# Optimization experiments

Hardware: AMD Instinct MI355X
Metric: run time of the kernel (lower is better)

The kernel has to match this reference:

```python
import jax, jax.numpy as jnp
import numpy as np

CHUNK = 64


def _rmsnorm(x, g, eps=1e-6):
    return x * jax.lax.rsqrt(jnp.mean(x * x, axis=-1, keepdims=True) + eps) * g


def setup_inputs() -> dict:
    key = jax.random.key(0)
    ks = jax.random.split(key, 8)
    B, L, D, N = 4, 4096, 512, 64
    s = 0.02
    return {
        'x': jax.random.normal(ks[0], (B, L, D), jnp.float32),
        'A_log': -jnp.ones((D,), jnp.float32) * jnp.log(2.0),
        'dt_bias': jnp.log(jnp.expm1(jax.random.uniform(ks[1], (D,), jnp.float32, 0.001, 0.1))),
        'D_skip': jnp.ones((D,), jnp.float32),
        'W_xproj': jax.random.normal(ks[2], (D, 2 * D), jnp.float32) * s,
        'b_xproj': jnp.zeros((2 * D,), jnp.float32),
        'W_B': jax.random.normal(ks[3], (D, N), jnp.float32) * s,
        'W_C': jax.random.normal(ks[4], (D, N), jnp.float32) * s,
        'W_dt': jax.random.normal(ks[5], (D, D), jnp.float32) * s,
        'g_Bnorm': jnp.ones((N,), jnp.float32),
        'g_Cnorm': jnp.ones((N,), jnp.float32),
        'g_outnorm': jnp.ones((D,), jnp.float32),
        'W_out': jax.random.normal(ks[6], (D, D), jnp.float32) * s,
        'b_out': jnp.zeros((D,), jnp.float32),
    }


def reference(x, A_log, dt_bias, D_skip, W_xproj, b_xproj, W_B, W_C, W_dt,
              g_Bnorm, g_Cnorm, g_outnorm, W_out, b_out):
    b, l, d = x.shape
    n = W_B.shape[1]
    p = CHUNK
    c = l // p  # L chosen divisible by chunk size (original pads otherwise)

    A = -jnp.exp(jnp.clip(A_log, -20.0, 2.0))  # (d,)
    xp = x @ W_xproj + b_xproj                  # (b,l,2d)
    x_bar, z = jnp.split(xp, 2, axis=-1)
    Bm = _rmsnorm(x_bar @ W_B, g_Bnorm)         # (b,l,n)
    Cm = _rmsnorm(x_bar @ W_C, g_Cnorm)         # (b,l,n)
    dt = jnp.clip(jax.nn.softplus(x_bar @ W_dt + dt_bias), 1e-4, 5.0)
    A_bar = jnp.exp(jnp.clip(dt * A, -20.0, 0.0))  # (b,l,d)

    to_chunks = lambda t: t.reshape(b, c, p, t.shape[-1]).transpose(1, 0, 2, 3)
    xc, Bc, Cc, Ac = map(to_chunks, (x_bar, Bm, Cm, A_bar))  # (c,b,p,*)
    mask = jnp.tril(jnp.ones((p, p), x.dtype))

    def process_chunk(prev_state, inputs):
        x_c, B_c, C_c, A_c = inputs
        log_a = jnp.log(jnp.clip(A_c, 1e-8, 1.0))
        la_cs = jnp.cumsum(log_a, axis=1)  # (b,p,d)
        # intra-chunk decay matrix M: (b,p,p,d)
        M = jnp.exp(la_cs[:, :, None, :] - la_cs[:, None, :, :]) * mask[None, :, :, None]
        BX = jnp.einsum('bpn,bpd->bpnd', B_c, x_c)
        state = jnp.einsum('bijd,bjnd->bind', M, BX)
        y_intra = jnp.einsum('bpn,bpnd->bpd', C_c, state)
        decay = jnp.exp(la_cs)
        y_inter = jnp.einsum('bpn,bpnd->bpd', C_c,
                             prev_state[:, None, :, :] * decay[:, :, None, :])
        y_c = y_intra + y_inter
        a_total = jnp.exp(la_cs[:, -1, :])             # (b,d)
        a_to_end = jnp.exp(la_cs[:, -1:, :] - la_cs)   # (b,p,d)
        chunk_state = jnp.einsum('bpn,bpd->bnd', B_c, x_c * a_to_end)
        new_state = prev_state * a_total[:, None, :] + chunk_state
        new_state = jnp.where(jnp.isfinite(new_state), new_state, 0.0)
        y_c = jnp.where(jnp.isfinite(y_c), y_c, 0.0)
        return new_state, y_c

    init = jnp.zeros((b, n, d), x.dtype)
    _, yc = jax.lax.scan(jax.checkpoint(process_chunk), init, (xc, Bc, Cc, Ac))
    y = yc.transpose(1, 0, 2, 3).reshape(b, l, d)
    y = jnp.where(jnp.isfinite(y), y, 0.0)
    y = y + D_skip * x_bar
    y = _rmsnorm(y, g_outnorm) * jax.nn.silu(z)
    return y @ W_out + b_out
```

## Files before the change

kernel.cpp:

```cpp
#include <hip/hip_runtime.h>
#include <hip/hip_bf16.h>
#include <math.h>

typedef __hip_bfloat16 bf16;
typedef __attribute__((ext_vector_type(8))) short short8;
typedef __attribute__((ext_vector_type(4))) float floatx4;

#define B_ 4
#define L_ 4096
#define D_ 512
#define M_ (B_*L_)

__device__ __forceinline__ float b2f(bf16 v){ return __bfloat162float(v); }
__device__ __forceinline__ bf16  f2b(float v){ return __float2bfloat16(v); }
__device__ __forceinline__ short f2bs(float v){ bf16 h = __float2bfloat16(v); short s; __builtin_memcpy(&s,&h,2); return s; }

#define GLD16(gp, lp) __builtin_amdgcn_global_load_lds( \
    (const __attribute__((address_space(1))) void*)(gp), \
    (__attribute__((address_space(3))) void*)(lp), 16, 0, 0)

__global__ __launch_bounds__(1024) void k_transpose(const float* __restrict__ src,
                                                    bf16* __restrict__ dst, int K, int N){
    __shared__ float tile[32][33];
    int n0 = blockIdx.x*32, k0 = blockIdx.y*32;
    int tx = threadIdx.x, ty = threadIdx.y;
    tile[ty][tx] = src[(size_t)(k0+ty)*N + n0+tx];
    __syncthreads();
    ((short*)dst)[(size_t)(n0+ty)*K + k0+tx] = f2bs(tile[tx][ty]);
}

__global__ __launch_bounds__(256) void k_cvt(const float* __restrict__ src,
                                             bf16* __restrict__ dst){
    size_t i = ((size_t)blockIdx.x*256 + threadIdx.x)*4;
    float4 v = *(const float4*)(src + i);
    short4 s; s.x=f2bs(v.x); s.y=f2bs(v.y); s.z=f2bs(v.z); s.w=f2bs(v.w);
    *(short4*)((short*)dst + i) = s;
}

template<int EPI>
__global__ __launch_bounds__(256) void k_gemm(const bf16* __restrict__ Ap,
        const bf16* __restrict__ Wt, const float* __restrict__ bias,
        const float* __restrict__ aux,
        float* __restrict__ o1, bf16* __restrict__ o2, bf16* __restrict__ o3){
    __shared__ short As[128*32];
    __shared__ short Bs[128*32];
    const int K = 512;
    int m0 = blockIdx.x*128, n0 = blockIdx.y*128;
    int tid=threadIdx.x, w=tid>>6, lane=tid&63;
    int wr=w>>1, wc=w&1, quad=lane>>4, r16=lane&15;
    floatx4 acc[4][4];
    #pragma unroll
    for (int i=0;i<4;i++)
        #pragma unroll
        for (int j=0;j<4;j++)
            #pragma unroll
            for (int e=0;e<4;e++) acc[i][j][e]=0.f;

    int c0 = tid, c1 = tid + 256;
    const short* Ab = (const short*)Ap + (size_t)m0*K;
    const short* Wb = (const short*)Wt + (size_t)n0*K;
    int r0 = c0>>2, g0 = (c0&3)*8;
    int r1 = c1>>2, g1 = (c1&3)*8;

    for (int k0=0;k0<K;k0+=32){
        GLD16(Ab + (size_t)r0*K + k0 + g0, &As[c0*8]);
        GLD16(Ab + (size_t)r1*K + k0 + g1, &As[c1*8]);
        GLD16(Wb + (size_t)r0*K + k0 + g0, &Bs[c0*8]);
        GLD16(Wb + (size_t)r1*K + k0 + g1, &Bs[c1*8]);
        __syncthreads();
        short8 af[4], bv[4];
        #pragma unroll
        for (int i=0;i<4;i++) af[i] = *(short8*)&As[(wr*64+i*16+r16)*32 + quad*8];
        #pragma unroll
        for (int j=0;j<4;j++) bv[j] = *(short8*)&Bs[(wc*64+j*16+r16)*32 + quad*8];
        #pragma unroll
        for (int i=0;i<4;i++)
            #pragma unroll
            for (int j=0;j<4;j++)
                acc[i][j] = __builtin_amdgcn_mfma_f32_16x16x32_bf16(af[i], bv[j], acc[i][j], 0,0,0);
        __syncthreads();
    }
    #pragma unroll
    for (int i=0;i<4;i++)
    #pragma unroll
    for (int j=0;j<4;j++)
    #pragma unroll
    for (int reg=0;reg<4;reg++){
        int gr = m0 + wr*64 + i*16 + quad*4 + reg;
        int gc = n0 + wc*64 + j*16 + r16;
        float v = acc[i][j][reg] + bias[gc];
        if (EPI==0){
            if (gc < 512){
                o1[(size_t)gr*512 + gc] = v;
                o2[(size_t)gr*512 + gc] = f2b(v);
            } else {
                o3[(size_t)gr*512 + (gc-512)] = f2b(v / (1.f + __expf(-v)));
            }
        } else if (EPI==1){
            float sp = (v > 15.f) ? v : log1pf(__expf(v));
            float dt = fminf(fmaxf(sp, 1e-4f), 5.f);
            float Ad = -__expf(fminf(fmaxf(aux[gc], -20.f), 2.f));
            o1[(size_t)gr*512 + gc] = fminf(fmaxf(dt*Ad, -18.420680743952367f), 0.f);
        } else {
            o1[(size_t)gr*512 + gc] = v;
        }
    }
}

__device__ __forceinline__ void gemm_tile_64x64(const bf16* __restrict__ Aptr,
                                                const bf16* __restrict__ Wt,
                                                int K, int m0, int n0,
                                                short (*As)[32], short (*Ns)[32],
                                                floatx4 acc[2][2]){
    int tid  = threadIdx.x;
    int w    = tid >> 6, lane = tid & 63;
    int wr   = w >> 1,  wc   = w & 1;
    int quad = lane >> 4, r16 = lane & 15;
    #pragma unroll
    for (int i=0;i<2;i++)
        #pragma unroll
        for (int j=0;j<2;j++)
            #pragma unroll
            for (int e=0;e<4;e++) acc[i][j][e] = 0.f;
    int lrow = tid >> 2, lkg = (tid & 3) * 8;
    for (int k0 = 0; k0 < K; k0 += 32){
        *(short8*)&As[lrow][lkg] = *(const short8*)((const short*)Aptr + (size_t)(m0+lrow)*K + k0 + lkg);
        *(short8*)&Ns[lrow][lkg] = *(const short8*)((const short*)Wt   + (size_t)(n0+lrow)*K + k0 + lkg);
        __syncthreads();
        short8 af[2], bfr[2];
        #pragma unroll
        for (int t=0;t<2;t++) af[t]  = *(short8*)&As[wr*32 + t*16 + r16][quad*8];
        #pragma unroll
        for (int t=0;t<2;t++) bfr[t] = *(short8*)&Ns[wc*32 + t*16 + r16][quad*8];
        #pragma unroll
        for (int i=0;i<2;i++)
            #pragma unroll
            for (int j=0;j<2;j++)
                acc[i][j] = __builtin_amdgcn_mfma_f32_16x16x32_bf16(af[i], bfr[j], acc[i][j], 0,0,0);
        __syncthreads();
    }
}

__global__ __launch_bounds__(256) void k_bcproj(const bf16* __restrict__ xbarh,
        const bf16* __restrict__ WtB, const bf16* __restrict__ WtC,
        const float* __restrict__ gB, const float* __restrict__ gC,
        float* __restrict__ Bm, float* __restrict__ Cm){
    __shared__ short As[64][32], Ns[64][32];
    __shared__ float Ls[64][64];
    __shared__ float rfac[64];
    const bf16* Wt = blockIdx.y ? WtC : WtB;
    const float* g = blockIdx.y ? gC  : gB;
    float* outp    = blockIdx.y ? Cm  : Bm;
    floatx4 acc[2][2];
    int m0 = blockIdx.x*64;
    gemm_tile_64x64(xbarh, Wt, 512, m0, 0, As, Ns, acc);
    int tid=threadIdx.x, w=tid>>6, lane=tid&63, wr=w>>1, wc=w&1, quad=lane>>4, r16=lane&15;
    #pragma unroll
    for (int i=0;i<2;i++)
    #pragma unroll
    for (int j=0;j<2;j++)
    #pragma unroll
    for (int reg=0;reg<4;reg++)
        Ls[wr*32+i*16+quad*4+reg][wc*32+j*16+r16] = acc[i][j][reg];
    __syncthreads();
    if (tid < 64){
        float ss = 0.f;
        #pragma unroll
        for (int cc=0;cc<64;cc++){ float t = Ls[tid][cc]; ss += t*t; }
        rfac[tid] = rsqrtf(ss*(1.f/64.f) + 1e-6f);
    }
    __syncthreads();
    #pragma unroll
    for (int it=0; it<16; it++){
        int idx = it*256 + tid;
        int r = idx >> 6, cc = idx & 63;
        outp[(size_t)(m0+r)*64 + cc] = Ls[r][cc] * rfac[r] * g[cc];
    }
}

__global__ __launch_bounds__(256) void k_pass1(const float* __restrict__ la,
        const float* __restrict__ xbar, const float* __restrict__ Bm,
        float* __restrict__ local, float* __restrict__ atot){
    __shared__ float Bs[64*64];
    int c=blockIdx.x, b=blockIdx.y, d=blockIdx.z*256+threadIdx.x;
    size_t rowbase=(size_t)b*L_+(size_t)c*64;
    size_t cb=(size_t)c*4+b;
    {
        const float4* src=(const float4*)(Bm + rowbase*64);
        float4* dst=(float4*)Bs;
        #pragma unroll
        for (int k=0;k<4;k++) dst[k*256+threadIdx.x]=src[k*256+threadIdx.x];
    }
    __syncthreads();
    float4 st[16];
    #pragma unroll
    for (int k=0;k<16;k++) st[k]=make_float4(0.f,0.f,0.f,0.f);
    float cs=0.f;
    size_t off0=rowbase*512+d;
    float la_n=la[off0], x_n=xbar[off0];
    #pragma unroll 2
    for (int i=0;i<64;i++){
        float lai=la_n, xi=x_n;
        if (i<63){ la_n=la[off0+(i+1)*512]; x_n=xbar[off0+(i+1)*512]; }
        float ai=__expf(lai);
        cs += lai;
        const float* Br=Bs+i*64;
        #pragma unroll
        for (int k=0;k<16;k++){
            float4 bv=*(const float4*)(Br+k*4);
            float4 s=st[k];
            s.x=fmaf(ai,s.x,bv.x*xi); s.y=fmaf(ai,s.y,bv.y*xi);
            s.z=fmaf(ai,s.z,bv.z*xi); s.w=fmaf(ai,s.w,bv.w*xi);
            st[k]=s;
        }
    }
    #pragma unroll
    for (int k=0;k<16;k++){
        size_t ob=(cb*64 + k*4)*512 + d;
        local[ob]      = st[k].x;
        local[ob+512]  = st[k].y;
        local[ob+1024] = st[k].z;
        local[ob+1536] = st[k].w;
    }
    atot[cb*512+d]=__expf(cs);
}

__global__ __launch_bounds__(256) void k_scan(float* __restrict__ local,
        const float* __restrict__ atot){
    int idx = blockIdx.x*256 + threadIdx.x;
    int d = idx & 511, n = (idx >> 9) & 63, b = idx >> 15;
    float s = 0.f;
    for (int c=0;c<64;c++){
        size_t cb = (size_t)c*4 + b;
        size_t off = (cb*64 + n)*512 + d;
        float v = local[off];
        local[off] = s;
        s = s * atot[cb*512 + d] + v;
        if (!isfinite(s)) s = 0.f;
    }
}

__global__ __launch_bounds__(256) void k_pass2(const float* __restrict__ la,
        const float* __restrict__ xbar, const float* __restrict__ Bm,
        const float* __restrict__ Cm, const float* __restrict__ Sprev,
        float* __restrict__ ybuf){
    __shared__ float Bs[64*64];
    __shared__ float Cs[64*64];
    int c=blockIdx.x, b=blockIdx.y, d=blockIdx.z*256+threadIdx.x;
    size_t rowbase=(size_t)b*L_+(size_t)c*64;
    size_t cb=(size_t)c*4+b;
    {
        const float4* sb=(const float4*)(Bm + rowbase*64);
        const float4* sc=(const float4*)(Cm + rowbase*64);
        float4* db=(float4*)Bs; float4* dc=(float4*)Cs;
        #pragma unroll
        for (int k=0;k<4;k++){
            db[k*256+threadIdx.x]=sb[k*256+threadIdx.x];
            dc[k*256+threadIdx.x]=sc[k*256+threadIdx.x];
        }
    }
    float4 st[16];
    #pragma unroll
    for (int k=0;k<16;k++){
        size_t ib=(cb*64 + k*4)*512 + d;
        st[k].x=Sprev[ib]; st[k].y=Sprev[ib+512];
        st[k].z=Sprev[ib+1024]; st[k].w=Sprev[ib+1536];
    }
    __syncthreads();
    size_t off0=rowbase*512+d;
    float la_n=la[off0], x_n=xbar[off0];
    #pragma unroll 2
    for (int i=0;i<64;i++){
        float lai=la_n, xi=x_n;
        if (i<63){ la_n=la[off0+(i+1)*512]; x_n=xbar[off0+(i+1)*512]; }
        float ai=__expf(lai);
        const float* Br=Bs+i*64;
        const float* Cr=Cs+i*64;
        float4 yv=make_float4(0.f,0.f,0.f,0.f);
        #pragma unroll
        for (int k=0;k<16;k++){
            float4 bv=*(const float4*)(Br+k*4);
            float4 cv=*(const float4*)(Cr+k*4);
            float4 s=st[k];
            s.x=fmaf(ai,s.x,bv.x*xi); s.y=fmaf(ai,s.y,bv.y*xi);
            s.z=fmaf(ai,s.z,bv.z*xi); s.w=fmaf(ai,s.w,bv.w*xi);
            st[k]=s;
            yv.x=fmaf(cv.x,s.x,yv.x); yv.y=fmaf(cv.y,s.y,yv.y);
            yv.z=fmaf(cv.z,s.z,yv.z); yv.w=fmaf(cv.w,s.w,yv.w);
        }
        float yo=(yv.x+yv.y)+(yv.z+yv.w);
        if (!isfinite(yo)) yo=0.f;
        ybuf[off0+i*512]=yo;
    }
}

__global__ __launch_bounds__(256) void k_outnorm(const float* __restrict__ y,
        const float* __restrict__ xbar, const float* __restrict__ Dskip,
        const float* __restrict__ g, const bf16* __restrict__ siluz,
        bf16* __restrict__ u){
    int wave = threadIdx.x >> 6, lane = threadIdx.x & 63;
    size_t row = (size_t)blockIdx.x*4 + wave;
    float v[8]; float ss = 0.f;
    #pragma unroll
    for (int j=0;j<8;j++){
        int d = j*64 + lane;
        float t = y[row*512 + d] + Dskip[d] * xbar[row*512 + d];
        v[j] = t; ss += t*t;
    }
    #pragma unroll
    for (int m=1;m<64;m<<=1) ss += __shfl_xor(ss, m, 64);
    float r = rsqrtf(ss*(1.f/512.f) + 1e-6f);
    #pragma unroll
    for (int j=0;j<8;j++){
        int d = j*64 + lane;
        u[row*512 + d] = f2b(v[j] * r * g[d] * b2f(siluz[row*512 + d]));
    }
}

extern "C" void kernel_launch(void* const* d_in, const int* in_sizes, int n_in,
                              void* d_out, int out_size, void* d_ws, size_t ws_size,
                              hipStream_t stream){
    const float* x       = (const float*)d_in[0];
    const float* A_log   = (const float*)d_in[1];
    const float* dt_bias = (const float*)d_in[2];
    const float* D_skip  = (const float*)d_in[3];
    const float* W_xproj = (const float*)d_in[4];
    const float* b_xproj = (const float*)d_in[5];
    const float* W_B     = (const float*)d_in[6];
    const float* W_C     = (const float*)d_in[7];
    const float* W_dt    = (const float*)d_in[8];
    const float* g_B     = (const float*)d_in[9];
    const float* g_C     = (const float*)d_in[10];
    const float* g_out   = (const float*)d_in[11];
    const float* W_out   = (const float*)d_in[12];
    const float* b_out   = (const float*)d_in[13];
    float* out = (float*)d_out;

    char* wp = (char*)d_ws;
    auto alloc = [&](size_t bytes)->char*{ char* p = wp; wp += (bytes + 255) & ~(size_t)255; return p; };
    float* xbar  = (float*)alloc((size_t)M_*512*4);
    bf16*  xh    = (bf16*) alloc((size_t)M_*512*2);
    bf16*  xbarh = (bf16*) alloc((size_t)M_*512*2);
    bf16*  siluz = (bf16*) alloc((size_t)M_*512*2);
    float* la    = (float*)alloc((size_t)M_*512*4);
    float* Bm    = (float*)alloc((size_t)M_*64*4);
    float* Cm    = (float*)alloc((size_t)M_*64*4);
    float* local = (float*)alloc((size_t)256*64*512*4);
    float* atot  = (float*)alloc((size_t)256*512*4);
    float* ybuf  = (float*)alloc((size_t)M_*512*4);
    bf16*  u     = (bf16*) alloc((size_t)M_*512*2);
    bf16*  WtX   = (bf16*) alloc((size_t)1024*512*2);
    bf16*  WtD   = (bf16*) alloc((size_t)512*512*2);
    bf16*  WtO   = (bf16*) alloc((size_t)512*512*2);
    bf16*  WtB   = (bf16*) alloc((size_t)64*512*2);
    bf16*  WtC   = (bf16*) alloc((size_t)64*512*2);

    dim3 tb(32,32);
    k_transpose<<<dim3(32,16), tb, 0, stream>>>(W_xproj, WtX, 512, 1024);
    k_transpose<<<dim3(16,16), tb, 0, stream>>>(W_dt,   WtD, 512, 512);
    k_transpose<<<dim3(16,16), tb, 0, stream>>>(W_out,  WtO, 512, 512);
    k_transpose<<<dim3(2,16),  tb, 0, stream>>>(W_B,    WtB, 512, 64);
    k_transpose<<<dim3(2,16),  tb, 0, stream>>>(W_C,    WtC, 512, 64);
    k_cvt      <<<M_*512/1024, 256, 0, stream>>>(x, xh);

    k_gemm<0> <<<dim3(128, 8), 256, 0, stream>>>(xh,    WtX, b_xproj, nullptr, xbar, xbarh, siluz);
    k_bcproj  <<<dim3(256, 2), 256, 0, stream>>>(xbarh, WtB, WtC, g_B, g_C, Bm, Cm);
    k_gemm<1> <<<dim3(128, 4), 256, 0, stream>>>(xbarh, WtD, dt_bias, A_log, la, nullptr, nullptr);
    k_pass1   <<<dim3(64,4,2), 256, 0, stream>>>(la, xbar, Bm, local, atot);
    k_scan    <<<512,          256, 0, stream>>>(local, atot);
    k_pass2   <<<dim3(64,4,2), 256, 0, stream>>>(la, xbar, Bm, Cm, local, ybuf);
    k_outnorm <<<M_/4,         256, 0, stream>>>(ybuf, xbar, D_skip, g_out, siluz, u);
    k_gemm<2> <<<dim3(128, 4), 256, 0, stream>>>(u,     WtO, b_out, nullptr, out, nullptr, nullptr);
}
```

Measured before the change: 372.4 us.

## Fuse B/C projections into main GEMM epilogue and pack two channels per scan thread

Replaces the separate 64x64-tile B/C projection kernel with one 128-wide GEMM launch over a concatenated B|C weight matrix. That launch applies both RMS norms in its epilogue using cross-lane shuffles. The chunk-scan pass1/pass2 kernels now give each thread two adjacent channels using float2 vectors, which halves the grid and doubles the state held in registers. This cuts launches and duplicate shared-memory loads of B/C, and may enable packed FP32 math. The cost is higher register pressure (128 state floats per thread) and half as many blocks in the scan kernels, which lowers occupancy.

```diff
diff --git a/kernel.cpp b/kernel.cpp
--- a/kernel.cpp
+++ b/kernel.cpp
@@ -5,6 +5,7 @@
 typedef __hip_bfloat16 bf16;
 typedef __attribute__((ext_vector_type(8))) short short8;
 typedef __attribute__((ext_vector_type(4))) float floatx4;
+typedef __attribute__((ext_vector_type(2))) float floatx2;
 
 #define B_ 4
 #define L_ 4096
@@ -14,6 +15,7 @@
 __device__ __forceinline__ float b2f(bf16 v){ return __bfloat162float(v); }
 __device__ __forceinline__ bf16  f2b(float v){ return __float2bfloat16(v); }
 __device__ __forceinline__ short f2bs(float v){ bf16 h = __float2bfloat16(v); short s; __builtin_memcpy(&s,&h,2); return s; }
+__device__ __forceinline__ floatx2 fx2(float v){ floatx2 r; r.x=v; r.y=v; return r; }
 
 #define GLD16(gp, lp) __builtin_amdgcn_global_load_lds( \
     (const __attribute__((address_space(1))) void*)(gp), \
@@ -41,7 +43,8 @@
 __global__ __launch_bounds__(256) void k_gemm(const bf16* __restrict__ Ap,
         const bf16* __restrict__ Wt, const float* __restrict__ bias,
         const float* __restrict__ aux,
-        float* __restrict__ o1, bf16* __restrict__ o2, bf16* __restrict__ o3){
+        float* __restrict__ o1, bf16* __restrict__ o2, bf16* __restrict__ o3,
+        float* __restrict__ o4){
     __shared__ short As[128*32];
     __shared__ short Bs[128*32];
     const int K = 512;
@@ -79,6 +82,29 @@
             for (int j=0;j<4;j++)
                 acc[i][j] = __builtin_amdgcn_mfma_f32_16x16x32_bf16(af[i], bv[j], acc[i][j], 0,0,0);
         __syncthreads();
+    }
+    if (EPI==3){
+        #pragma unroll
+        for (int i=0;i<4;i++)
+        #pragma unroll
+        for (int reg=0;reg<4;reg++){
+            float ss=0.f;
+            #pragma unroll
+            for (int j=0;j<4;j++){ float t=acc[i][j][reg]; ss+=t*t; }
+            #pragma unroll
+            for (int m=1;m<16;m<<=1) ss += __shfl_xor(ss, m, 64);
+            float rq = rsqrtf(ss*(1.f/64.f)+1e-6f);
+            int gr = m0 + wr*64 + i*16 + quad*4 + reg;
+            #pragma unroll
+            for (int j=0;j<4;j++){
+                int gc = wc*64 + j*16 + r16;
+                float gval = (gc<64) ? bias[gc] : aux[gc-64];
+                float v = acc[i][j][reg]*rq*gval;
+                if (gc<64) o1[(size_t)gr*64 + gc] = v;
+                else       o4[(size_t)gr*64 + (gc-64)] = v;
+            }
+        }
+        return;
     }
     #pragma unroll
     for (int i=0;i<4;i++)
@@ -107,82 +133,12 @@
     }
 }
 
-__device__ __forceinline__ void gemm_tile_64x64(const bf16* __restrict__ Aptr,
-                                                const bf16* __restrict__ Wt,
-                                                int K, int m0, int n0,
-                                                short (*As)[32], short (*Ns)[32],
-                                                floatx4 acc[2][2]){
-    int tid  = threadIdx.x;
-    int w    = tid >> 6, lane = tid & 63;
-    int wr   = w >> 1,  wc   = w & 1;
-    int quad = lane >> 4, r16 = lane & 15;
-    #pragma unroll
-    for (int i=0;i<2;i++)
-        #pragma unroll
-        for (int j=0;j<2;j++)
-            #pragma unroll
-            for (int e=0;e<4;e++) acc[i][j][e] = 0.f;
-    int lrow = tid >> 2, lkg = (tid & 3) * 8;
-    for (int k0 = 0; k0 < K; k0 += 32){
-        *(short8*)&As[lrow][lkg] = *(const short8*)((const short*)Aptr + (size_t)(m0+lrow)*K + k0 + lkg);
-        *(short8*)&Ns[lrow][lkg] = *(const short8*)((const short*)Wt   + (size_t)(n0+lrow)*K + k0 + lkg);
-        __syncthreads();
-        short8 af[2], bfr[2];
-        #pragma unroll
-        for (int t=0;t<2;t++) af[t]  = *(short8*)&As[wr*32 + t*16 + r16][quad*8];
-        #pragma unroll
-        for (int t=0;t<2;t++) bfr[t] = *(short8*)&Ns[wc*32 + t*16 + r16][quad*8];
-        #pragma unroll
-        for (int i=0;i<2;i++)
-            #pragma unroll
-            for (int j=0;j<2;j++)
-                acc[i][j] = __builtin_amdgcn_mfma_f32_16x16x32_bf16(af[i], bfr[j], acc[i][j], 0,0,0);
-        __syncthreads();
-    }
-}
-
-__global__ __launch_bounds__(256) void k_bcproj(const bf16* __restrict__ xbarh,
-        const bf16* __restrict__ WtB, const bf16* __restrict__ WtC,
-        const float* __restrict__ gB, const float* __restrict__ gC,
-        float* __restrict__ Bm, float* __restrict__ Cm){
-    __shared__ short As[64][32], Ns[64][32];
-    __shared__ float Ls[64][64];
-    __shared__ float rfac[64];
-    const bf16* Wt = blockIdx.y ? WtC : WtB;
-    const float* g = blockIdx.y ? gC  : gB;
-    float* outp    = blockIdx.y ? Cm  : Bm;
-    floatx4 acc[2][2];
-    int m0 = blockIdx.x*64;
-    gemm_tile_64x64(xbarh, Wt, 512, m0, 0, As, Ns, acc);
-    int tid=threadIdx.x, w=tid>>6, lane=tid&63, wr=w>>1, wc=w&1, quad=lane>>4, r16=lane&15;
-    #pragma unroll
-    for (int i=0;i<2;i++)
-    #pragma unroll
-    for (int j=0;j<2;j++)
-    #pragma unroll
-    for (int reg=0;reg<4;reg++)
-        Ls[wr*32+i*16+quad*4+reg][wc*32+j*16+r16] = acc[i][j][reg];
-    __syncthreads();
-    if (tid < 64){
-        float ss = 0.f;
-        #pragma unroll
-        for (int cc=0;cc<64;cc++){ float t = Ls[tid][cc]; ss += t*t; }
-        rfac[tid] = rsqrtf(ss*(1.f/64.f) + 1e-6f);
-    }
-    __syncthreads();
-    #pragma unroll
-    for (int it=0; it<16; it++){
-        int idx = it*256 + tid;
-        int r = idx >> 6, cc = idx & 63;
-        outp[(size_t)(m0+r)*64 + cc] = Ls[r][cc] * rfac[r] * g[cc];
-    }
-}
-
 __global__ __launch_bounds__(256) void k_pass1(const float* __restrict__ la,
         const float* __restrict__ xbar, const float* __restrict__ Bm,
         float* __restrict__ local, float* __restrict__ atot){
     __shared__ float Bs[64*64];
-    int c=blockIdx.x, b=blockIdx.y, d=blockIdx.z*256+threadIdx.x;
+    int c=blockIdx.x, b=blockIdx.y;
+    int d = threadIdx.x*2;
     size_t rowbase=(size_t)b*L_+(size_t)c*64;
     size_t cb=(size_t)c*4+b;
     {
@@ -192,37 +148,34 @@
         for (int k=0;k<4;k++) dst[k*256+threadIdx.x]=src[k*256+threadIdx.x];
     }
     __syncthreads();
-    float4 st[16];
-    #pragma unroll
-    for (int k=0;k<16;k++) st[k]=make_float4(0.f,0.f,0.f,0.f);
-    float cs=0.f;
+    floatx2 st[64];
+    #pragma unroll
+    for (int n=0;n<64;n++) st[n]=fx2(0.f);
+    floatx2 cs=fx2(0.f);
     size_t off0=rowbase*512+d;
-    float la_n=la[off0], x_n=xbar[off0];
+    floatx2 la_n=*(const floatx2*)(la+off0), x_n=*(const floatx2*)(xbar+off0);
     #pragma unroll 2
     for (int i=0;i<64;i++){
-        float lai=la_n, xi=x_n;
-        if (i<63){ la_n=la[off0+(i+1)*512]; x_n=xbar[off0+(i+1)*512]; }
-        float ai=__expf(lai);
-        cs += lai;
+        floatx2 lai=la_n, xi=x_n;
+        if (i<63){ la_n=*(const floatx2*)(la+off0+(i+1)*512);
+                   x_n =*(const floatx2*)(xbar+off0+(i+1)*512); }
+        floatx2 ai; ai.x=__expf(lai.x); ai.y=__expf(lai.y);
+        cs = cs + lai;
         const float* Br=Bs+i*64;
         #pragma unroll
         for (int k=0;k<16;k++){
             float4 bv=*(const float4*)(Br+k*4);
-            float4 s=st[k];
-            s.x=fmaf(ai,s.x,bv.x*xi); s.y=fmaf(ai,s.y,bv.y*xi);
-            s.z=fmaf(ai,s.z,bv.z*xi); s.w=fmaf(ai,s.w,bv.w*xi);
-            st[k]=s;
-        }
-    }
-    #pragma unroll
-    for (int k=0;k<16;k++){
-        size_t ob=(cb*64 + k*4)*512 + d;
-        local[ob]      = st[k].x;
-        local[ob+512]  = st[k].y;
-        local[ob+1024] = st[k].z;
-        local[ob+1536] = st[k].w;
-    }
-    atot[cb*512+d]=__expf(cs);
+            st[k*4+0]=ai*st[k*4+0]+fx2(bv.x)*xi;
+            st[k*4+1]=ai*st[k*4+1]+fx2(bv.y)*xi;
+            st[k*4+2]=ai*st[k*4+2]+fx2(bv.z)*xi;
+            st[k*4+3]=ai*st[k*4+3]+fx2(bv.w)*xi;
+        }
+    }
+    #pragma unroll
+    for (int n=0;n<64;n++)
+        *(floatx2*)(local + (cb*64+n)*512 + d) = st[n];
+    floatx2 at; at.x=__expf(cs.x); at.y=__expf(cs.y);
+    *(floatx2*)(atot + cb*512 + d) = at;
 }
 
 __global__ __launch_bounds__(256) void k_scan(float* __restrict__ local,
@@ -246,7 +199,8 @@
         float* __restrict__ ybuf){
     __shared__ float Bs[64*64];
     __shared__ float Cs[64*64];
-    int c=blockIdx.x, b=blockIdx.y, d=blockIdx.z*256+threadIdx.x;
+    int c=blockIdx.x, b=blockIdx.y;
+    int d = threadIdx.x*2;
     size_t rowbase=(size_t)b*L_+(size_t)c*64;
     size_t cb=(size_t)c*4+b;
     {
@@ -259,38 +213,35 @@
             dc[k*256+threadIdx.x]=sc[k*256+threadIdx.x];
         }
     }
-    float4 st[16];
-    #pragma unroll
-    for (int k=0;k<16;k++){
-        size_t ib=(cb*64 + k*4)*512 + d;
-        st[k].x=Sprev[ib]; st[k].y=Sprev[ib+512];
-        st[k].z=Sprev[ib+1024]; st[k].w=Sprev[ib+1536];
-    }
+    floatx2 st[64];
+    #pragma unroll
+    for (int n=0;n<64;n++)
+        st[n] = *(const floatx2*)(Sprev + (cb*64+n)*512 + d);
     __syncthreads();
     size_t off0=rowbase*512+d;
-    float la_n=la[off0], x_n=xbar[off0];
+    floatx2 la_n=*(const floatx2*)(la+off0), x_n=*(const floatx2*)(xbar+off0);
     #pragma unroll 2
     for (int i=0;i<64;i++){
-        float lai=la_n, xi=x_n;
-        if (i<63){ la_n=la[off0+(i+1)*512]; x_n=xbar[off0+(i+1)*512]; }
-        float ai=__expf(lai);
+        floatx2 lai=la_n, xi=x_n;
+        if (i<63){ la_n=*(const floatx2*)(la+off0+(i+1)*512);
+                   x_n =*(const floatx2*)(xbar+off0+(i+1)*512); }
+        floatx2 ai; ai.x=__expf(lai.x); ai.y=__expf(lai.y);
         const float* Br=Bs+i*64;
         const float* Cr=Cs+i*64;
-        float4 yv=make_float4(0.f,0.f,0.f,0.f);
+        floatx2 yv=fx2(0.f);
         #pragma unroll
         for (int k=0;k<16;k++){
             float4 bv=*(const float4*)(Br+k*4);
             float4 cv=*(const float4*)(Cr+k*4);
-            float4 s=st[k];
-            s.x=fmaf(ai,s.x,bv.x*xi); s.y=fmaf(ai,s.y,bv.y*xi);
-            s.z=fmaf(ai,s.z,bv.z*xi); s.w=fmaf(ai,s.w,bv.w*xi);
-            st[k]=s;
-            yv.x=fmaf(cv.x,s.x,yv.x); yv.y=fmaf(cv.y,s.y,yv.y);
-            yv.z=fmaf(cv.z,s.z,yv.z); yv.w=fmaf(cv.w,s.w,yv.w);
-        }
-        float yo=(yv.x+yv.y)+(yv.z+yv.w);
-        if (!isfinite(yo)) yo=0.f;
-        ybuf[off0+i*512]=yo;
+            floatx2 s;
+            s=ai*st[k*4+0]+fx2(bv.x)*xi; st[k*4+0]=s; yv=yv+fx2(cv.x)*s;
+            s=ai*st[k*4+1]+fx2(bv.y)*xi; st[k*4+1]=s; yv=yv+fx2(cv.y)*s;
+            s=ai*st[k*4+2]+fx2(bv.z)*xi; st[k*4+2]=s; yv=yv+fx2(cv.z)*s;
+            s=ai*st[k*4+3]+fx2(bv.w)*xi; st[k*4+3]=s; yv=yv+fx2(cv.w)*s;
+        }
+        if (!isfinite(yv.x)) yv.x=0.f;
+        if (!isfinite(yv.y)) yv.y=0.f;
+        *(floatx2*)(ybuf + off0 + (size_t)i*512) = yv;
     }
 }
 
@@ -352,23 +303,22 @@
     bf16*  WtX   = (bf16*) alloc((size_t)1024*512*2);
     bf16*  WtD   = (bf16*) alloc((size_t)512*512*2);
     bf16*  WtO   = (bf16*) alloc((size_t)512*512*2);
-    bf16*  WtB   = (bf16*) alloc((size_t)64*512*2);
-    bf16*  WtC   = (bf16*) alloc((size_t)64*512*2);
+    bf16*  WtBC  = (bf16*) alloc((size_t)128*512*2);
 
     dim3 tb(32,32);
     k_transpose<<<dim3(32,16), tb, 0, stream>>>(W_xproj, WtX, 512, 1024);
     k_transpose<<<dim3(16,16), tb, 0, stream>>>(W_dt,   WtD, 512, 512);
     k_transpose<<<dim3(16,16), tb, 0, stream>>>(W_out,  WtO, 512, 512);
-    k_transpose<<<dim3(2,16),  tb, 0, stream>>>(W_B,    WtB, 512, 64);
-    k_transpose<<<dim3(2,16),  tb, 0, stream>>>(W_C,    WtC, 512, 64);
+    k_transpose<<<dim3(2,16),  tb, 0, stream>>>(W_B,    WtBC,          512, 64);
+    k_transpose<<<dim3(2,16),  tb, 0, stream>>>(W_C,    WtBC+64*512,   512, 64);
     k_cvt      <<<M_*512/1024, 256, 0, stream>>>(x, xh);
 
-    k_gemm<0> <<<dim3(128, 8), 256, 0, stream>>>(xh,    WtX, b_xproj, nullptr, xbar, xbarh, siluz);
-    k_bcproj  <<<dim3(256, 2), 256, 0, stream>>>(xbarh, WtB, WtC, g_B, g_C, Bm, Cm);
-    k_gemm<1> <<<dim3(128, 4), 256, 0, stream>>>(xbarh, WtD, dt_bias, A_log, la, nullptr, nullptr);
-    k_pass1   <<<dim3(64,4,2), 256, 0, stream>>>(la, xbar, Bm, local, atot);
+    k_gemm<0> <<<dim3(128, 8), 256, 0, stream>>>(xh,    WtX,  b_xproj, nullptr, xbar, xbarh, siluz, nullptr);
+    k_gemm<3> <<<dim3(128, 1), 256, 0, stream>>>(xbarh, WtBC, g_B, g_C, Bm, nullptr, nullptr, Cm);
+    k_gemm<1> <<<dim3(128, 4), 256, 0, stream>>>(xbarh, WtD,  dt_bias, A_log, la, nullptr, nullptr, nullptr);
+    k_pass1   <<<dim3(64, 4),  256, 0, stream>>>(la, xbar, Bm, local, atot);
     k_scan    <<<512,          256, 0, stream>>>(local, atot);
-    k_pass2   <<<dim3(64,4,2), 256, 0, stream>>>(la, xbar, Bm, Cm, local, ybuf);
+    k_pass2   <<<dim3(64, 4),  256, 0, stream>>>(la, xbar, Bm, Cm, local, ybuf);
     k_outnorm <<<M_/4,         256, 0, stream>>>(ybuf, xbar, D_skip, g_out, siluz, u);
-    k_gemm<2> <<<dim3(128, 4), 256, 0, stream>>>(u,     WtO, b_out, nullptr, out, nullptr, nullptr);
-}
+    k_gemm<2> <<<dim3(128, 4), 256, 0, stream>>>(u,     WtO,  b_out, nullptr, out, nullptr, nullptr, nullptr);
+}
```

Measured after the change: 375.5 us. About the same (+0.8%).
